# Kernel optimization log

Hardware: AMD Instinct MI355X
Metric: run time of the kernel (lower is better)

## Reference

```python
import jax, jax.numpy as jnp
import numpy as np

DIM = 512
HEADS = 8
EPS = 1e-5


def layer_norm(x, g, b):
    mu = jnp.mean(x, axis=-1, keepdims=True)
    var = jnp.mean(jnp.square(x - mu), axis=-1, keepdims=True)
    return (x - mu) * jax.lax.rsqrt(var + EPS) * g + b


def setup_inputs() -> dict:
    key = jax.random.key(0)
    ks = jax.random.split(key, 8)
    d = DIM
    s = 0.02
    return {
        "x": jax.random.normal(ks[0], (2, d, 64, 64), jnp.float32),
        "ln1_g": jnp.ones((d,), jnp.float32),
        "ln1_b": jnp.zeros((d,), jnp.float32),
        "w_qkv": jax.random.normal(ks[1], (d, 3 * d), jnp.float32) * s,
        "b_qkv": jnp.zeros((3 * d,), jnp.float32),
        "w_proj": jax.random.normal(ks[2], (d, d), jnp.float32) * s,
        "b_proj": jnp.zeros((d,), jnp.float32),
        "ln2_g": jnp.ones((d,), jnp.float32),
        "ln2_b": jnp.zeros((d,), jnp.float32),
        "w_ffn1": jax.random.normal(ks[3], (d, 4 * d), jnp.float32) * s,
        "b_ffn1": jnp.zeros((4 * d,), jnp.float32),
        "w_ffn2": jax.random.normal(ks[4], (4 * d, d), jnp.float32) * s,
        "b_ffn2": jnp.zeros((d,), jnp.float32),
    }


def reference(x, ln1_g, ln1_b, w_qkv, b_qkv, w_proj, b_proj,
              ln2_g, ln2_b, w_ffn1, b_ffn1, w_ffn2, b_ffn2):
    B, C, H, W = x.shape
    hd = C // HEADS
    x_in = x
    t = x.reshape(B, C, H * W).transpose(0, 2, 1)  # [B, N, C]
    h = layer_norm(t, ln1_g, ln1_b)
    qkv = h @ w_qkv + b_qkv  # [B, N, 3C]
    q, k, v = jnp.split(qkv, 3, axis=-1)
    def to_heads(a):
        return a.reshape(B, -1, HEADS, hd).transpose(0, 2, 1, 3)  # [B, h, N, hd]
    q, k, v = to_heads(q), to_heads(k), to_heads(v)
    # NOTE: module scales by 1/sqrt(C), not 1/sqrt(head_dim)
    attn = jnp.einsum('bhqd,bhkd->bhqk', q, k) / jnp.sqrt(jnp.float32(C))
    attn = jax.nn.softmax(attn, axis=-1)
    out = jnp.einsum('bhqk,bhkd->bhqd', attn, v)
    out = out.transpose(0, 2, 1, 3).reshape(B, -1, C)
    out = out @ w_proj + b_proj
    t = t + out
    h2 = layer_norm(t, ln2_g, ln2_b)
    ffn = jax.nn.relu(h2 @ w_ffn1 + b_ffn1) @ w_ffn2 + b_ffn2
    t = t + ffn
    y = t.transpose(0, 2, 1).reshape(B, C, H, W)
    return y + x_in
```

## Files before the change

kernel.cpp:

```cpp
#include <hip/hip_runtime.h>
#include <hip/hip_bf16.h>

typedef __bf16 bf16;
typedef __bf16 bf16x8 __attribute__((ext_vector_type(8)));
typedef __bf16 bf16x4 __attribute__((ext_vector_type(4)));
typedef float f32x4 __attribute__((ext_vector_type(4)));
typedef int int4v __attribute__((ext_vector_type(4)));
typedef int int2v __attribute__((ext_vector_type(2)));

#define DEV static __device__ __forceinline__

DEV void gload16(const void* g, void* l) {
    __builtin_amdgcn_global_load_lds(
        (const __attribute__((address_space(1))) void*)g,
        (__attribute__((address_space(3))) void*)l, 16, 0, 0);
}

DEV f32x4 mfma16(bf16x8 a, bf16x8 b, f32x4 c) {
    return __builtin_amdgcn_mfma_f32_16x16x32_bf16(a, b, c, 0, 0, 0);
}

DEV int cvtpk(float lo, float hi) {
    int r;
    asm("v_cvt_pk_bf16_f32 %0, %1, %2" : "=v"(r) : "v"(lo), "v"(hi));
    return r;
}

DEV float rexp2(float x) {
    float r;
    asm("v_exp_f32 %0, %1" : "=v"(r) : "v"(x));
    return r;
}

__global__ __launch_bounds__(256)
void k_transpose_x(const float* __restrict__ x, float* __restrict__ t) {
    __shared__ float tile[32][33];
    int bid = blockIdx.x;
    int nt = bid & 127, ct = (bid >> 7) & 15, b = bid >> 11;
    int n0 = nt * 32, c0 = ct * 32;
    int tid = threadIdx.x;
    const float* xb = x + (size_t)b * 512 * 4096;
    int nl = tid & 31, cl = tid >> 5;
#pragma unroll
    for (int i = 0; i < 4; i++) {
        int c = cl + i * 8;
        tile[c][nl] = xb[(size_t)(c0 + c) * 4096 + n0 + nl];
    }
    __syncthreads();
    float* tb = t + (size_t)b * 4096 * 512;
    int cl2 = tid & 31, nl2 = tid >> 5;
#pragma unroll
    for (int i = 0; i < 4; i++) {
        int n = nl2 + i * 8;
        tb[(size_t)(n0 + n) * 512 + c0 + cl2] = tile[cl2][n];
    }
}

__global__ __launch_bounds__(256)
void k_out3(const float* __restrict__ t, const bf16* __restrict__ f2o,
            const float* __restrict__ x, float* __restrict__ y) {
    __shared__ float tile[32][33];
    int bid = blockIdx.x;
    int nt = bid & 127, ct = (bid >> 7) & 15, b = bid >> 11;
    int n0 = nt * 32, c0 = ct * 32;
    int tid = threadIdx.x;
#pragma unroll
    for (int i = 0; i < 4; i++) {
        int nl = (tid >> 5) + i * 8;
        size_t idx = (size_t)(b * 4096 + n0 + nl) * 512 + c0 + (tid & 31);
        tile[tid & 31][nl] = t[idx] + (float)f2o[idx];
    }
    __syncthreads();
    const float* xb = x + ((size_t)b * 512 + c0) * 4096;
    float* yb = y + ((size_t)b * 512 + c0) * 4096;
#pragma unroll
    for (int i = 0; i < 4; i++) {
        int cl = (tid >> 5) + i * 8;
        int nl = tid & 31;
        size_t off = (size_t)cl * 4096 + n0 + nl;
        yb[off] = tile[cl][nl] + xb[off];
    }
}

__global__ __launch_bounds__(256)
void k_ln(const float* __restrict__ t, const float* __restrict__ gg,
          const float* __restrict__ bb, bf16* __restrict__ h) {
    int lane = threadIdx.x & 63;
    int row = blockIdx.x * 4 + (threadIdx.x >> 6);
    const float* tr = t + (size_t)row * 512;
    f32x4 v0 = *(const f32x4*)(tr + lane * 4);
    f32x4 v1 = *(const f32x4*)(tr + 256 + lane * 4);
    float s = v0[0] + v0[1] + v0[2] + v0[3] + v1[0] + v1[1] + v1[2] + v1[3];
#pragma unroll
    for (int m = 1; m < 64; m <<= 1) s += __shfl_xor(s, m);
    float mu = s * (1.0f / 512.0f);
    float vs = 0.f;
#pragma unroll
    for (int j = 0; j < 4; j++) {
        float d0 = v0[j] - mu, d1 = v1[j] - mu;
        vs += d0 * d0 + d1 * d1;
    }
#pragma unroll
    for (int m = 1; m < 64; m <<= 1) vs += __shfl_xor(vs, m);
    float rs = rsqrtf(vs * (1.0f / 512.0f) + 1e-5f);
    f32x4 g0 = *(const f32x4*)(gg + lane * 4);
    f32x4 g1 = *(const f32x4*)(gg + 256 + lane * 4);
    f32x4 b0 = *(const f32x4*)(bb + lane * 4);
    f32x4 b1 = *(const f32x4*)(bb + 256 + lane * 4);
    bf16x4 o0, o1;
#pragma unroll
    for (int j = 0; j < 4; j++) {
        o0[j] = (bf16)((v0[j] - mu) * rs * g0[j] + b0[j]);
        o1[j] = (bf16)((v1[j] - mu) * rs * g1[j] + b1[j]);
    }
    *(bf16x4*)(h + (size_t)row * 512 + lane * 4) = o0;
    *(bf16x4*)(h + (size_t)row * 512 + 256 + lane * 4) = o1;
}

__global__ __launch_bounds__(256)
void k_lnr(float* __restrict__ t, const bf16* __restrict__ r,
           const float* __restrict__ gg, const float* __restrict__ bb,
           bf16* __restrict__ h) {
    int lane = threadIdx.x & 63;
    int row = blockIdx.x * 4 + (threadIdx.x >> 6);
    float* tr = t + (size_t)row * 512;
    f32x4 v0 = *(const f32x4*)(tr + lane * 4);
    f32x4 v1 = *(const f32x4*)(tr + 256 + lane * 4);
    bf16x4 r0 = *(const bf16x4*)(r + (size_t)row * 512 + lane * 4);
    bf16x4 r1 = *(const bf16x4*)(r + (size_t)row * 512 + 256 + lane * 4);
#pragma unroll
    for (int j = 0; j < 4; j++) {
        v0[j] += (float)r0[j];
        v1[j] += (float)r1[j];
    }
    *(f32x4*)(tr + lane * 4) = v0;
    *(f32x4*)(tr + 256 + lane * 4) = v1;
    float s = v0[0] + v0[1] + v0[2] + v0[3] + v1[0] + v1[1] + v1[2] + v1[3];
#pragma unroll
    for (int m = 1; m < 64; m <<= 1) s += __shfl_xor(s, m);
    float mu = s * (1.0f / 512.0f);
    float vs = 0.f;
#pragma unroll
    for (int j = 0; j < 4; j++) {
        float d0 = v0[j] - mu, d1 = v1[j] - mu;
        vs += d0 * d0 + d1 * d1;
    }
#pragma unroll
    for (int m = 1; m < 64; m <<= 1) vs += __shfl_xor(vs, m);
    float rs = rsqrtf(vs * (1.0f / 512.0f) + 1e-5f);
    f32x4 g0 = *(const f32x4*)(gg + lane * 4);
    f32x4 g1 = *(const f32x4*)(gg + 256 + lane * 4);
    f32x4 b0 = *(const f32x4*)(bb + lane * 4);
    f32x4 b1 = *(const f32x4*)(bb + 256 + lane * 4);
    bf16x4 o0, o1;
#pragma unroll
    for (int j = 0; j < 4; j++) {
        o0[j] = (bf16)((v0[j] - mu) * rs * g0[j] + b0[j]);
        o1[j] = (bf16)((v1[j] - mu) * rs * g1[j] + b1[j]);
    }
    *(bf16x4*)(h + (size_t)row * 512 + lane * 4) = o0;
    *(bf16x4*)(h + (size_t)row * 512 + 256 + lane * 4) = o1;
}

__global__ __launch_bounds__(256)
void k_wt(const float* __restrict__ w, bf16* __restrict__ wt, int K, int N) {
    __shared__ float tile[32][33];
    int ntn = N >> 5;
    int kt = blockIdx.x / ntn, ntile = blockIdx.x % ntn;
    int k0 = kt * 32, n0 = ntile * 32;
    int tid = threadIdx.x;
    int nl = tid & 31, kl = tid >> 5;
#pragma unroll
    for (int i = 0; i < 4; i++) {
        int k = kl + i * 8;
        tile[k][nl] = w[(size_t)(k0 + k) * N + n0 + nl];
    }
    __syncthreads();
    int kl2 = tid & 31, nl2 = tid >> 5;
#pragma unroll
    for (int i = 0; i < 4; i++) {
        int n = nl2 + i * 8;
        wt[(size_t)(n0 + n) * K + k0 + kl2] = (bf16)tile[kl2][n];
    }
}

template <int MODE>
__global__ __launch_bounds__(256, 2)
void k_gemm(const bf16* __restrict__ A, const bf16* __restrict__ BT,
            const float* __restrict__ bias, bf16* __restrict__ outb,
            bf16* __restrict__ vtout, int M, int N, int K) {
    __shared__ char smem[65536];
    int ntn = N >> 7;
    int nwg = gridDim.x;
    int bid = blockIdx.x;
    int cpx = nwg >> 3;
    bid = (bid & 7) * cpx + (bid >> 3);
    int bm = bid / ntn, bn = bid % ntn;
    int m0 = bm * 128, n0 = bn * 128;
    int tid = threadIdx.x;
    int w = tid >> 6, l = tid & 63;
    int wm = w >> 1, wn = w & 1;
    int l15 = l & 15, lg = l >> 4;

    f32x4 acc[4][4];
#pragma unroll
    for (int i = 0; i < 4; i++)
#pragma unroll
        for (int j = 0; j < 4; j++) acc[i][j] = (f32x4){0.f, 0.f, 0.f, 0.f};

    int srow = tid >> 3, sphys = tid & 7;
    int lrow_a = wm * 64 + l15;
    int lrow_b = wn * 64 + l15;

#define GEMM_STAGE(k0v, bb)                                                  \
    do {                                                                     \
        _Pragma("unroll") for (int s = 0; s < 4; s++) {                      \
            int row = s * 32 + srow;                                         \
            int k16 = sphys ^ (row & 7);                                     \
            gload16(A + (size_t)(m0 + row) * K + (k0v) + k16 * 8,            \
                    smem + (bb) * 16384 + s * 4096 + tid * 16);              \
            gload16(BT + (size_t)(n0 + row) * K + (k0v) + k16 * 8,           \
                    smem + 32768 + (bb) * 16384 + s * 4096 + tid * 16);      \
        }                                                                    \
    } while (0)

    int nk = K >> 6;
    GEMM_STAGE(0, 0);
    int cur = 0;
    for (int kt = 0; kt < nk; kt++) {
        if (kt + 1 < nk) {
            GEMM_STAGE((kt + 1) << 6, cur ^ 1);
            asm volatile("s_waitcnt vmcnt(8)" ::: "memory");
        } else {
            asm volatile("s_waitcnt vmcnt(0)" ::: "memory");
        }
        __builtin_amdgcn_s_barrier();
        __builtin_amdgcn_sched_barrier(0);
        const char* pA = smem + cur * 16384;
        const char* pB = smem + 32768 + cur * 16384;
#pragma unroll
        for (int ks = 0; ks < 2; ks++) {
            bf16x8 af[4], bfr[4];
#pragma unroll
            for (int rg = 0; rg < 4; rg++) {
                int row = lrow_a + rg * 16;
                af[rg] = *(const bf16x8*)(pA + row * 128 +
                                          (((lg + ks * 4) ^ (row & 7)) << 4));
            }
#pragma unroll
            for (int cg = 0; cg < 4; cg++) {
                int row = lrow_b + cg * 16;
                bfr[cg] = *(const bf16x8*)(pB + row * 128 +
                                           (((lg + ks * 4) ^ (row & 7)) << 4));
            }
#pragma unroll
            for (int rg = 0; rg < 4; rg++)
#pragma unroll
                for (int cg = 0; cg < 4; cg++)
                    acc[rg][cg] = mfma16(af[rg], bfr[cg], acc[rg][cg]);
        }
        __builtin_amdgcn_s_barrier();
        cur ^= 1;
    }
#undef GEMM_STAGE

    if (MODE == 2 && n0 >= 1024) {
        char* vl = smem;
#pragma unroll
        for (int cg = 0; cg < 4; cg++) {
            int col = wn * 64 + cg * 16 + l15;
            float bz = bias[n0 + col];
#pragma unroll
            for (int rg = 0; rg < 4; rg++) {
                int rowb = wm * 64 + rg * 16 + lg * 4;
                int2v qq = {cvtpk(acc[rg][cg][0] + bz, acc[rg][cg][1] + bz),
                            cvtpk(acc[rg][cg][2] + bz, acc[rg][cg][3] + bz)};
                *(int2v*)(vl + col * 272 + rowb * 2) = qq;
            }
        }
        __syncthreads();
        int b = m0 >> 12, nrow0 = m0 & 4095;
        int dl = tid >> 3, c8 = tid & 7;
#pragma unroll
        for (int dd = 0; dd < 4; dd++) {
            int d = dd * 32 + dl;
            int ch = (n0 - 1024) + d;
            bf16* dst = vtout +
                ((size_t)((b * 8 + (ch >> 6)) * 64 + (ch & 63))) * 4096 + nrow0;
#pragma unroll
            for (int half = 0; half < 2; half++) {
                int chunk = half * 8 + c8;
                bf16x8 vv = *(const bf16x8*)(vl + d * 272 + chunk * 16);
                *(bf16x8*)(dst + chunk * 8) = vv;
            }
        }
        return;
    }

    char* ep = smem;
#pragma unroll
    for (int cg = 0; cg < 4; cg++) {
        int lcol = wn * 64 + cg * 16 + l15;
        float bz = bias[n0 + lcol];
#pragma unroll
        for (int rg = 0; rg < 4; rg++) {
#pragma unroll
            for (int j = 0; j < 4; j++) {
                int lrow = wm * 64 + rg * 16 + lg * 4 + j;
                float v = acc[rg][cg][j] + bz;
                if (MODE == 1) v = fmaxf(v, 0.f);
                *(bf16*)(ep + lrow * 264 + lcol * 2) = (bf16)v;
            }
        }
    }
    __syncthreads();
    int cch = tid & 15, rof = tid >> 4;
#pragma unroll
    for (int i = 0; i < 8; i++) {
        int row = i * 16 + rof;
        bf16x8 vv = *(const bf16x8*)(ep + row * 264 + cch * 16);
        *(bf16x8*)(outb + (size_t)(m0 + row) * N + n0 + cch * 8) = vv;
    }
}

__global__ __launch_bounds__(256, 4)
void k_attn(const bf16* __restrict__ qkvb, const bf16* __restrict__ vt,
            bf16* __restrict__ attno) {
    __shared__ bf16 sK[2][64 * 64];
    __shared__ bf16 sV[2][64 * 64];
    const float sc = 0.044194173824159216f * 1.4426950408889634f;
    int bid = blockIdx.x;
    int nb = (bid & 7) * 128 + (bid >> 3);
    int bh = nb >> 6, qt = nb & 63;
    int b = bh >> 3, hh = bh & 7;
    int q0 = qt * 64;
    int tid = threadIdx.x, w = tid >> 6, l = tid & 63;
    int l15 = l & 15, lg = l >> 4, l7 = l15 & 7;
    int lg4 = lg * 4;
    int vperm = ((lg & 1) << 1) | (lg >> 1);
    const bf16* qbase = qkvb + (size_t)b * 4096 * 1536 + hh * 64;
    const bf16* kbase = qbase + 512;
    const bf16* vbase = vt + (size_t)bh * 64 * 4096;
    int srow = tid >> 3, sphys = tid & 7;

    const char* kp0 = (const char*)&sK[0][0] + l15 * 128 + ((lg ^ l7) << 4);
    const char* kp1 = (const char*)&sK[0][0] + l15 * 128 + (((4 + lg) ^ l7) << 4);
    const char* vp0 = (const char*)&sV[0][0] + l15 * 128 + ((vperm ^ l7) << 4);
    const char* vp1 = (const char*)&sV[0][0] + l15 * 128 + (((4 + vperm) ^ l7) << 4);
    char* dK0 = (char*)&sK[0][0] + tid * 16;
    char* dV0 = (char*)&sV[0][0] + tid * 16;
    const char* kg = (const char*)(kbase + srow * 1536 + (sphys ^ (srow & 7)) * 8);
    const char* vg = (const char*)(vbase + srow * 4096 + (sphys ^ (srow & 7)) * 8);

    gload16(kg, dK0);
    gload16(kg + 98304, dK0 + 4096);
    gload16(vg, dV0);
    gload16(vg + 262144, dV0 + 4096);
    kg += 196608;
    vg += 128;

    bf16x8 qf[2];
#pragma unroll
    for (int ks = 0; ks < 2; ks++) {
        bf16x8 v = *(const bf16x8*)(qbase +
            (size_t)(q0 + w * 16 + l15) * 1536 + ks * 32 + lg * 8);
        bf16x8 o;
#pragma unroll
        for (int j = 0; j < 8; j++) o[j] = (bf16)((float)v[j] * sc);
        qf[ks] = o;
    }

    float lsum = 0.f;
    f32x4 acc[4];
#pragma unroll
    for (int df = 0; df < 4; df++) acc[df] = (f32x4){0.f, 0.f, 0.f, 0.f};

#define ABODY(BUF, PF)                                                        \
    {                                                                         \
        if (PF) {                                                             \
            gload16(kg, dK0 + (1 - (BUF)) * 8192);                            \
            gload16(kg + 98304, dK0 + (1 - (BUF)) * 8192 + 4096);             \
            gload16(vg, dV0 + (1 - (BUF)) * 8192);                            \
            gload16(vg + 262144, dV0 + (1 - (BUF)) * 8192 + 4096);            \
            kg += 196608;                                                     \
            vg += 128;                                                        \
            asm volatile("s_waitcnt vmcnt(4)" ::: "memory");                  \
        } else {                                                              \
            asm volatile("s_waitcnt vmcnt(0)" ::: "memory");                  \
        }                                                                     \
        __builtin_amdgcn_s_barrier();                                         \
        __builtin_amdgcn_sched_barrier(0);                                    \
        f32x4 s0 = {0.f, 0.f, 0.f, 0.f}, s1 = s0, s2 = s0, s3 = s0;           \
        __builtin_amdgcn_s_setprio(1);                                        \
        s0 = mfma16(*(const bf16x8*)(kp0 + (BUF) * 8192 + 0 * 2048), qf[0], s0); \
        s1 = mfma16(*(const bf16x8*)(kp0 + (BUF) * 8192 + 1 * 2048), qf[0], s1); \
        s2 = mfma16(*(const bf16x8*)(kp0 + (BUF) * 8192 + 2 * 2048), qf[0], s2); \
        s3 = mfma16(*(const bf16x8*)(kp0 + (BUF) * 8192 + 3 * 2048), qf[0], s3); \
        s0 = mfma16(*(const bf16x8*)(kp1 + (BUF) * 8192 + 0 * 2048), qf[1], s0); \
        s1 = mfma16(*(const bf16x8*)(kp1 + (BUF) * 8192 + 1 * 2048), qf[1], s1); \
        s2 = mfma16(*(const bf16x8*)(kp1 + (BUF) * 8192 + 2 * 2048), qf[1], s2); \
        s3 = mfma16(*(const bf16x8*)(kp1 + (BUF) * 8192 + 3 * 2048), qf[1], s3); \
        __builtin_amdgcn_s_setprio(0);                                        \
        float e0 = rexp2(s0[0]), e1 = rexp2(s0[1]);                           \
        float e2 = rexp2(s0[2]), e3 = rexp2(s0[3]);                           \
        float e4 = rexp2(s1[0]), e5 = rexp2(s1[1]);                           \
        float e6 = rexp2(s1[2]), e7 = rexp2(s1[3]);                           \
        float e8 = rexp2(s2[0]), e9 = rexp2(s2[1]);                           \
        float e10 = rexp2(s2[2]), e11 = rexp2(s2[3]);                         \
        float e12 = rexp2(s3[0]), e13 = rexp2(s3[1]);                         \
        float e14 = rexp2(s3[2]), e15 = rexp2(s3[3]);                         \
        lsum += (((e0 + e1) + (e2 + e3)) + ((e4 + e5) + (e6 + e7))) +         \
                (((e8 + e9) + (e10 + e11)) + ((e12 + e13) + (e14 + e15)));    \
        int p0 = cvtpk(e0, e1), p1 = cvtpk(e2, e3);                           \
        int p2 = cvtpk(e4, e5), p3 = cvtpk(e6, e7);                           \
        int p4 = cvtpk(e8, e9), p5 = cvtpk(e10, e11);                         \
        int p6 = cvtpk(e12, e13), p7 = cvtpk(e14, e15);                       \
        asm("v_permlane16_swap_b32 %0, %1" : "+v"(p2), "+v"(p0));             \
        asm("v_permlane16_swap_b32 %0, %1" : "+v"(p3), "+v"(p1));             \
        asm("v_permlane16_swap_b32 %0, %1" : "+v"(p6), "+v"(p4));             \
        asm("v_permlane16_swap_b32 %0, %1" : "+v"(p7), "+v"(p5));             \
        {                                                                     \
            int4v ai = {p0, p1, p2, p3};                                      \
            bf16x8 af = __builtin_bit_cast(bf16x8, ai);                       \
            __builtin_amdgcn_s_setprio(1);                                    \
            acc[0] = mfma16(af, *(const bf16x8*)(vp0 + (BUF) * 8192 + 0 * 2048), acc[0]); \
            acc[1] = mfma16(af, *(const bf16x8*)(vp0 + (BUF) * 8192 + 1 * 2048), acc[1]); \
            acc[2] = mfma16(af, *(const bf16x8*)(vp0 + (BUF) * 8192 + 2 * 2048), acc[2]); \
            acc[3] = mfma16(af, *(const bf16x8*)(vp0 + (BUF) * 8192 + 3 * 2048), acc[3]); \
        }                                                                     \
        {                                                                     \
            int4v ai = {p4, p5, p6, p7};                                      \
            bf16x8 af = __builtin_bit_cast(bf16x8, ai);                       \
            acc[0] = mfma16(af, *(const bf16x8*)(vp1 + (BUF) * 8192 + 0 * 2048), acc[0]); \
            acc[1] = mfma16(af, *(const bf16x8*)(vp1 + (BUF) * 8192 + 1 * 2048), acc[1]); \
            acc[2] = mfma16(af, *(const bf16x8*)(vp1 + (BUF) * 8192 + 2 * 2048), acc[2]); \
            acc[3] = mfma16(af, *(const bf16x8*)(vp1 + (BUF) * 8192 + 3 * 2048), acc[3]); \
            __builtin_amdgcn_s_setprio(0);                                    \
        }                                                                     \
        __builtin_amdgcn_s_barrier();                                         \
    }

    for (int tt = 0; tt < 31; tt++) {
        ABODY(0, 1)
        ABODY(1, 1)
    }
    ABODY(0, 1)
    ABODY(1, 0)
#undef ABODY

    lsum += __shfl_xor(lsum, 16);
    lsum += __shfl_xor(lsum, 32);
    float invq[4];
#pragma unroll
    for (int j = 0; j < 4; j++)
        invq[j] = 1.0f / __shfl(lsum, lg4 + j);

    bf16* ow = (bf16*)&sK[0][0] + w * 16 * 64;
#pragma unroll
    for (int df = 0; df < 4; df++) {
        int chunk = df * 2 + (l15 >> 3);
        int within = l15 & 7;
#pragma unroll
        for (int j = 0; j < 4; j++) {
            int q = lg * 4 + j;
            *(bf16*)((char*)ow + q * 128 + ((chunk ^ (q & 7)) << 4) + within * 2) =
                (bf16)(acc[df][j] * invq[j]);
        }
    }
    __syncthreads();
    const char* owr = (const char*)ow;
#pragma unroll
    for (int half = 0; half < 2; half++) {
        int r = l >> 2, ch = (l & 3) + half * 4;
        bf16x8 vv = *(const bf16x8*)(owr + r * 128 + ((ch ^ (r & 7)) << 4));
        *(bf16x8*)(attno + (size_t)(b * 4096 + q0 + w * 16 + r) * 512 +
                   hh * 64 + ch * 8) = vv;
    }
}

extern "C" void kernel_launch(void* const* d_in, const int* in_sizes, int n_in,
                              void* d_out, int out_size, void* d_ws, size_t ws_size,
                              hipStream_t stream) {
    const float* x = (const float*)d_in[0];
    const float* ln1g = (const float*)d_in[1];
    const float* ln1b = (const float*)d_in[2];
    const float* wqkv = (const float*)d_in[3];
    const float* bqkv = (const float*)d_in[4];
    const float* wproj = (const float*)d_in[5];
    const float* bproj = (const float*)d_in[6];
    const float* ln2g = (const float*)d_in[7];
    const float* ln2b = (const float*)d_in[8];
    const float* wffn1 = (const float*)d_in[9];
    const float* bffn1 = (const float*)d_in[10];
    const float* wffn2 = (const float*)d_in[11];
    const float* bffn2 = (const float*)d_in[12];
    float* y = (float*)d_out;

    char* ws = (char*)d_ws;
    float* t    = (float*)(ws + 0);
    bf16* h     = (bf16*)(ws + 16777216);
    bf16* qkvb  = (bf16*)(ws + 25165824);
    bf16* vtb   = (bf16*)(ws + 50331648);
    bf16* f1    = (bf16*)(ws + 25165824);
    bf16* wqT   = (bf16*)(ws + 58720256);
    bf16* wpT   = (bf16*)(ws + 60293120);
    bf16* w1T   = (bf16*)(ws + 60817408);
    bf16* w2T   = (bf16*)(ws + 62914560);
    bf16* attno = h;
    bf16* po    = vtb;
    bf16* f2o   = h;

    k_transpose_x<<<4096, 256, 0, stream>>>(x, t);
    k_ln<<<2048, 256, 0, stream>>>(t, ln1g, ln1b, h);
    k_wt<<<(512 / 32) * (1536 / 32), 256, 0, stream>>>(wqkv, wqT, 512, 1536);
    k_wt<<<(512 / 32) * (512 / 32), 256, 0, stream>>>(wproj, wpT, 512, 512);
    k_wt<<<(512 / 32) * (2048 / 32), 256, 0, stream>>>(wffn1, w1T, 512, 2048);
    k_wt<<<(2048 / 32) * (512 / 32), 256, 0, stream>>>(wffn2, w2T, 2048, 512);

    k_gemm<2><<<768, 256, 0, stream>>>(h, wqT, bqkv, qkvb, vtb, 8192, 1536, 512);
    k_attn<<<1024, 256, 0, stream>>>(qkvb, vtb, attno);
    k_gemm<0><<<256, 256, 0, stream>>>(attno, wpT, bproj, po, nullptr, 8192, 512, 512);
    k_lnr<<<2048, 256, 0, stream>>>(t, po, ln2g, ln2b, h);
    k_gemm<1><<<1024, 256, 0, stream>>>(h, w1T, bffn1, f1, nullptr, 8192, 2048, 512);
    k_gemm<0><<<256, 256, 0, stream>>>(f1, w2T, bffn2, f2o, nullptr, 8192, 512, 2048);
    k_out3<<<4096, 256, 0, stream>>>(t, f2o, x, y);
}
```

Measured before the change: 203.7 us.

## Triple-buffer attention with software-pipelined QK and 64-wide GEMM tiles for N=512

The attention kernel moves to a three-stage LDS ring and software-pipelines the loop, so the QK^T MFMAs for tile i+1 are issued before the softmax and PV of tile i. This lets exp work overlap with matrix work and keeps two prefetches in flight. Occupancy drops from 4 to 3 blocks per CU because of the larger shared buffer. Separately, the GEMM gains a BN template parameter, and the two N=512 GEMMs use 128x64 tiles with twice the workgroups, to fill the CUs better with only 256 tiles.

```diff
diff --git a/kernel.cpp b/kernel.cpp
--- a/kernel.cpp
+++ b/kernel.cpp
@@ -184,33 +184,34 @@
     }
 }
 
-template <int MODE>
+template <int MODE, int BN>
 __global__ __launch_bounds__(256, 2)
 void k_gemm(const bf16* __restrict__ A, const bf16* __restrict__ BT,
             const float* __restrict__ bias, bf16* __restrict__ outb,
             bf16* __restrict__ vtout, int M, int N, int K) {
     __shared__ char smem[65536];
-    int ntn = N >> 7;
+    constexpr int CG = BN / 32;
+    int ntn = N / BN;
     int nwg = gridDim.x;
     int bid = blockIdx.x;
     int cpx = nwg >> 3;
     bid = (bid & 7) * cpx + (bid >> 3);
     int bm = bid / ntn, bn = bid % ntn;
-    int m0 = bm * 128, n0 = bn * 128;
+    int m0 = bm * 128, n0 = bn * BN;
     int tid = threadIdx.x;
     int w = tid >> 6, l = tid & 63;
     int wm = w >> 1, wn = w & 1;
     int l15 = l & 15, lg = l >> 4;
 
-    f32x4 acc[4][4];
+    f32x4 acc[4][CG];
 #pragma unroll
     for (int i = 0; i < 4; i++)
 #pragma unroll
-        for (int j = 0; j < 4; j++) acc[i][j] = (f32x4){0.f, 0.f, 0.f, 0.f};
+        for (int j = 0; j < CG; j++) acc[i][j] = (f32x4){0.f, 0.f, 0.f, 0.f};
 
     int srow = tid >> 3, sphys = tid & 7;
     int lrow_a = wm * 64 + l15;
-    int lrow_b = wn * 64 + l15;
+    int lrow_b = wn * (BN / 2) + l15;
 
 #define GEMM_STAGE(k0v, bb)                                                  \
     do {                                                                     \
@@ -219,6 +220,10 @@
             int k16 = sphys ^ (row & 7);                                     \
             gload16(A + (size_t)(m0 + row) * K + (k0v) + k16 * 8,            \
                     smem + (bb) * 16384 + s * 4096 + tid * 16);              \
+        }                                                                    \
+        _Pragma("unroll") for (int s = 0; s < CG; s++) {                     \
+            int row = s * 32 + srow;                                         \
+            int k16 = sphys ^ (row & 7);                                     \
             gload16(BT + (size_t)(n0 + row) * K + (k0v) + k16 * 8,           \
                     smem + 32768 + (bb) * 16384 + s * 4096 + tid * 16);      \
         }                                                                    \
@@ -230,7 +235,10 @@
     for (int kt = 0; kt < nk; kt++) {
         if (kt + 1 < nk) {
             GEMM_STAGE((kt + 1) << 6, cur ^ 1);
-            asm volatile("s_waitcnt vmcnt(8)" ::: "memory");
+            if constexpr (BN == 128)
+                asm volatile("s_waitcnt vmcnt(8)" ::: "memory");
+            else
+                asm volatile("s_waitcnt vmcnt(6)" ::: "memory");
         } else {
             asm volatile("s_waitcnt vmcnt(0)" ::: "memory");
         }
@@ -240,7 +248,7 @@
         const char* pB = smem + 32768 + cur * 16384;
 #pragma unroll
         for (int ks = 0; ks < 2; ks++) {
-            bf16x8 af[4], bfr[4];
+            bf16x8 af[4], bfr[CG];
 #pragma unroll
             for (int rg = 0; rg < 4; rg++) {
                 int row = lrow_a + rg * 16;
@@ -248,7 +256,7 @@
                                           (((lg + ks * 4) ^ (row & 7)) << 4));
             }
 #pragma unroll
-            for (int cg = 0; cg < 4; cg++) {
+            for (int cg = 0; cg < CG; cg++) {
                 int row = lrow_b + cg * 16;
                 bfr[cg] = *(const bf16x8*)(pB + row * 128 +
                                            (((lg + ks * 4) ^ (row & 7)) << 4));
@@ -256,7 +264,7 @@
 #pragma unroll
             for (int rg = 0; rg < 4; rg++)
 #pragma unroll
-                for (int cg = 0; cg < 4; cg++)
+                for (int cg = 0; cg < CG; cg++)
                     acc[rg][cg] = mfma16(af[rg], bfr[cg], acc[rg][cg]);
         }
         __builtin_amdgcn_s_barrier();
@@ -264,43 +272,47 @@
     }
 #undef GEMM_STAGE
 
-    if (MODE == 2 && n0 >= 1024) {
-        char* vl = smem;
-#pragma unroll
-        for (int cg = 0; cg < 4; cg++) {
-            int col = wn * 64 + cg * 16 + l15;
-            float bz = bias[n0 + col];
-#pragma unroll
-            for (int rg = 0; rg < 4; rg++) {
-                int rowb = wm * 64 + rg * 16 + lg * 4;
-                int2v qq = {cvtpk(acc[rg][cg][0] + bz, acc[rg][cg][1] + bz),
-                            cvtpk(acc[rg][cg][2] + bz, acc[rg][cg][3] + bz)};
-                *(int2v*)(vl + col * 272 + rowb * 2) = qq;
+    if constexpr (MODE == 2) {
+        if (n0 >= 1024) {
+            char* vl = smem;
+#pragma unroll
+            for (int cg = 0; cg < CG; cg++) {
+                int col = wn * 64 + cg * 16 + l15;
+                float bz = bias[n0 + col];
+#pragma unroll
+                for (int rg = 0; rg < 4; rg++) {
+                    int rowb = wm * 64 + rg * 16 + lg * 4;
+                    int2v qq = {cvtpk(acc[rg][cg][0] + bz, acc[rg][cg][1] + bz),
+                                cvtpk(acc[rg][cg][2] + bz, acc[rg][cg][3] + bz)};
+                    *(int2v*)(vl + col * 272 + rowb * 2) = qq;
+                }
             }
+            __syncthreads();
+            int b = m0 >> 12, nrow0 = m0 & 4095;
+            int dl = tid >> 3, c8 = tid & 7;
+#pragma unroll
+            for (int dd = 0; dd < 4; dd++) {
+                int d = dd * 32 + dl;
+                int ch = (n0 - 1024) + d;
+                bf16* dst = vtout +
+                    ((size_t)((b * 8 + (ch >> 6)) * 64 + (ch & 63))) * 4096 + nrow0;
+#pragma unroll
+                for (int half = 0; half < 2; half++) {
+                    int chunk = half * 8 + c8;
+                    bf16x8 vv = *(const bf16x8*)(vl + d * 272 + chunk * 16);
+                    *(bf16x8*)(dst + chunk * 8) = vv;
+                }
+            }
+            return;
         }
-        __syncthreads();
-        int b = m0 >> 12, nrow0 = m0 & 4095;
-        int dl = tid >> 3, c8 = tid & 7;
-#pragma unroll
-        for (int dd = 0; dd < 4; dd++) {
-            int d = dd * 32 + dl;
-            int ch = (n0 - 1024) + d;
-            bf16* dst = vtout +
-                ((size_t)((b * 8 + (ch >> 6)) * 64 + (ch & 63))) * 4096 + nrow0;
-#pragma unroll
-            for (int half = 0; half < 2; half++) {
-                int chunk = half * 8 + c8;
-                bf16x8 vv = *(const bf16x8*)(vl + d * 272 + chunk * 16);
-                *(bf16x8*)(dst + chunk * 8) = vv;
-            }
-        }
-        return;
-    }
-
+    }
+
+    constexpr int RS = BN * 2 + 8;
+    constexpr int CH = BN / 8;
     char* ep = smem;
 #pragma unroll
-    for (int cg = 0; cg < 4; cg++) {
-        int lcol = wn * 64 + cg * 16 + l15;
+    for (int cg = 0; cg < CG; cg++) {
+        int lcol = wn * (BN / 2) + cg * 16 + l15;
         float bz = bias[n0 + lcol];
 #pragma unroll
         for (int rg = 0; rg < 4; rg++) {
@@ -309,25 +321,26 @@
                 int lrow = wm * 64 + rg * 16 + lg * 4 + j;
                 float v = acc[rg][cg][j] + bz;
                 if (MODE == 1) v = fmaxf(v, 0.f);
-                *(bf16*)(ep + lrow * 264 + lcol * 2) = (bf16)v;
+                *(bf16*)(ep + lrow * RS + lcol * 2) = (bf16)v;
             }
         }
     }
     __syncthreads();
-    int cch = tid & 15, rof = tid >> 4;
-#pragma unroll
-    for (int i = 0; i < 8; i++) {
-        int row = i * 16 + rof;
-        bf16x8 vv = *(const bf16x8*)(ep + row * 264 + cch * 16);
+    int cch = tid & (CH - 1);
+    int rof = tid / CH;
+    constexpr int RPP = 256 / CH;
+#pragma unroll
+    for (int i = 0; i < 128 / RPP; i++) {
+        int row = i * RPP + rof;
+        bf16x8 vv = *(const bf16x8*)(ep + row * RS + cch * 16);
         *(bf16x8*)(outb + (size_t)(m0 + row) * N + n0 + cch * 8) = vv;
     }
 }
 
-__global__ __launch_bounds__(256, 4)
+__global__ __launch_bounds__(256, 3)
 void k_attn(const bf16* __restrict__ qkvb, const bf16* __restrict__ vt,
             bf16* __restrict__ attno) {
-    __shared__ bf16 sK[2][64 * 64];
-    __shared__ bf16 sV[2][64 * 64];
+    __shared__ char sL[49152];
     const float sc = 0.044194173824159216f * 1.4426950408889634f;
     int bid = blockIdx.x;
     int nb = (bid & 7) * 128 + (bid >> 3);
@@ -343,21 +356,14 @@
     const bf16* vbase = vt + (size_t)bh * 64 * 4096;
     int srow = tid >> 3, sphys = tid & 7;
 
-    const char* kp0 = (const char*)&sK[0][0] + l15 * 128 + ((lg ^ l7) << 4);
-    const char* kp1 = (const char*)&sK[0][0] + l15 * 128 + (((4 + lg) ^ l7) << 4);
-    const char* vp0 = (const char*)&sV[0][0] + l15 * 128 + ((vperm ^ l7) << 4);
-    const char* vp1 = (const char*)&sV[0][0] + l15 * 128 + (((4 + vperm) ^ l7) << 4);
-    char* dK0 = (char*)&sK[0][0] + tid * 16;
-    char* dV0 = (char*)&sV[0][0] + tid * 16;
+    const char* kp0 = sL + l15 * 128 + ((lg ^ l7) << 4);
+    const char* kp1 = sL + l15 * 128 + (((4 + lg) ^ l7) << 4);
+    const char* vp0 = sL + 8192 + l15 * 128 + ((vperm ^ l7) << 4);
+    const char* vp1 = sL + 8192 + l15 * 128 + (((4 + vperm) ^ l7) << 4);
+    char* dK = sL + tid * 16;
+    char* dV = sL + 8192 + tid * 16;
     const char* kg = (const char*)(kbase + srow * 1536 + (sphys ^ (srow & 7)) * 8);
     const char* vg = (const char*)(vbase + srow * 4096 + (sphys ^ (srow & 7)) * 8);
-
-    gload16(kg, dK0);
-    gload16(kg + 98304, dK0 + 4096);
-    gload16(vg, dV0);
-    gload16(vg + 262144, dV0 + 4096);
-    kg += 196608;
-    vg += 128;
 
     bf16x8 qf[2];
 #pragma unroll
@@ -369,46 +375,50 @@
         for (int j = 0; j < 8; j++) o[j] = (bf16)((float)v[j] * sc);
         qf[ks] = o;
     }
-
+    asm volatile("s_waitcnt vmcnt(0)" ::: "memory");
+
+#define STG(BS)                                                               \
+    do {                                                                      \
+        gload16(kg, dK + (BS) * 16384);                                       \
+        gload16(kg + 98304, dK + (BS) * 16384 + 4096);                        \
+        gload16(vg, dV + (BS) * 16384);                                       \
+        gload16(vg + 262144, dV + (BS) * 16384 + 4096);                       \
+        kg += 196608;                                                         \
+        vg += 128;                                                            \
+    } while (0)
+
+    STG(0);
+    STG(1);
+
+    const f32x4 kZ = {0.f, 0.f, 0.f, 0.f};
+    f32x4 sE[4], sO[4];
     float lsum = 0.f;
     f32x4 acc[4];
 #pragma unroll
     for (int df = 0; df < 4; df++) acc[df] = (f32x4){0.f, 0.f, 0.f, 0.f};
 
-#define ABODY(BUF, PF)                                                        \
+#define QKC(SN, BQ)                                                           \
+    __builtin_amdgcn_s_setprio(1);                                            \
+    SN[0] = mfma16(*(const bf16x8*)(kp0 + (BQ) * 16384 + 0 * 2048), qf[0], kZ); \
+    SN[1] = mfma16(*(const bf16x8*)(kp0 + (BQ) * 16384 + 1 * 2048), qf[0], kZ); \
+    SN[2] = mfma16(*(const bf16x8*)(kp0 + (BQ) * 16384 + 2 * 2048), qf[0], kZ); \
+    SN[3] = mfma16(*(const bf16x8*)(kp0 + (BQ) * 16384 + 3 * 2048), qf[0], kZ); \
+    SN[0] = mfma16(*(const bf16x8*)(kp1 + (BQ) * 16384 + 0 * 2048), qf[1], SN[0]); \
+    SN[1] = mfma16(*(const bf16x8*)(kp1 + (BQ) * 16384 + 1 * 2048), qf[1], SN[1]); \
+    SN[2] = mfma16(*(const bf16x8*)(kp1 + (BQ) * 16384 + 2 * 2048), qf[1], SN[2]); \
+    SN[3] = mfma16(*(const bf16x8*)(kp1 + (BQ) * 16384 + 3 * 2048), qf[1], SN[3]); \
+    __builtin_amdgcn_s_setprio(0);
+
+#define SOFTPV(SOld, BP)                                                      \
     {                                                                         \
-        if (PF) {                                                             \
-            gload16(kg, dK0 + (1 - (BUF)) * 8192);                            \
-            gload16(kg + 98304, dK0 + (1 - (BUF)) * 8192 + 4096);             \
-            gload16(vg, dV0 + (1 - (BUF)) * 8192);                            \
-            gload16(vg + 262144, dV0 + (1 - (BUF)) * 8192 + 4096);            \
-            kg += 196608;                                                     \
-            vg += 128;                                                        \
-            asm volatile("s_waitcnt vmcnt(4)" ::: "memory");                  \
-        } else {                                                              \
-            asm volatile("s_waitcnt vmcnt(0)" ::: "memory");                  \
-        }                                                                     \
-        __builtin_amdgcn_s_barrier();                                         \
-        __builtin_amdgcn_sched_barrier(0);                                    \
-        f32x4 s0 = {0.f, 0.f, 0.f, 0.f}, s1 = s0, s2 = s0, s3 = s0;           \
-        __builtin_amdgcn_s_setprio(1);                                        \
-        s0 = mfma16(*(const bf16x8*)(kp0 + (BUF) * 8192 + 0 * 2048), qf[0], s0); \
-        s1 = mfma16(*(const bf16x8*)(kp0 + (BUF) * 8192 + 1 * 2048), qf[0], s1); \
-        s2 = mfma16(*(const bf16x8*)(kp0 + (BUF) * 8192 + 2 * 2048), qf[0], s2); \
-        s3 = mfma16(*(const bf16x8*)(kp0 + (BUF) * 8192 + 3 * 2048), qf[0], s3); \
-        s0 = mfma16(*(const bf16x8*)(kp1 + (BUF) * 8192 + 0 * 2048), qf[1], s0); \
-        s1 = mfma16(*(const bf16x8*)(kp1 + (BUF) * 8192 + 1 * 2048), qf[1], s1); \
-        s2 = mfma16(*(const bf16x8*)(kp1 + (BUF) * 8192 + 2 * 2048), qf[1], s2); \
-        s3 = mfma16(*(const bf16x8*)(kp1 + (BUF) * 8192 + 3 * 2048), qf[1], s3); \
-        __builtin_amdgcn_s_setprio(0);                                        \
-        float e0 = rexp2(s0[0]), e1 = rexp2(s0[1]);                           \
-        float e2 = rexp2(s0[2]), e3 = rexp2(s0[3]);                           \
-        float e4 = rexp2(s1[0]), e5 = rexp2(s1[1]);                           \
-        float e6 = rexp2(s1[2]), e7 = rexp2(s1[3]);                           \
-        float e8 = rexp2(s2[0]), e9 = rexp2(s2[1]);                           \
-        float e10 = rexp2(s2[2]), e11 = rexp2(s2[3]);                         \
-        float e12 = rexp2(s3[0]), e13 = rexp2(s3[1]);                         \
-        float e14 = rexp2(s3[2]), e15 = rexp2(s3[3]);                         \
+        float e0 = rexp2(SOld[0][0]), e1 = rexp2(SOld[0][1]);                 \
+        float e2 = rexp2(SOld[0][2]), e3 = rexp2(SOld[0][3]);                 \
+        float e4 = rexp2(SOld[1][0]), e5 = rexp2(SOld[1][1]);                 \
+        float e6 = rexp2(SOld[1][2]), e7 = rexp2(SOld[1][3]);                 \
+        float e8 = rexp2(SOld[2][0]), e9 = rexp2(SOld[2][1]);                 \
+        float e10 = rexp2(SOld[2][2]), e11 = rexp2(SOld[2][3]);               \
+        float e12 = rexp2(SOld[3][0]), e13 = rexp2(SOld[3][1]);               \
+        float e14 = rexp2(SOld[3][2]), e15 = rexp2(SOld[3][3]);               \
         lsum += (((e0 + e1) + (e2 + e3)) + ((e4 + e5) + (e6 + e7))) +         \
                 (((e8 + e9) + (e10 + e11)) + ((e12 + e13) + (e14 + e15)));    \
         int p0 = cvtpk(e0, e1), p1 = cvtpk(e2, e3);                           \
@@ -423,30 +433,58 @@
             int4v ai = {p0, p1, p2, p3};                                      \
             bf16x8 af = __builtin_bit_cast(bf16x8, ai);                       \
             __builtin_amdgcn_s_setprio(1);                                    \
-            acc[0] = mfma16(af, *(const bf16x8*)(vp0 + (BUF) * 8192 + 0 * 2048), acc[0]); \
-            acc[1] = mfma16(af, *(const bf16x8*)(vp0 + (BUF) * 8192 + 1 * 2048), acc[1]); \
-            acc[2] = mfma16(af, *(const bf16x8*)(vp0 + (BUF) * 8192 + 2 * 2048), acc[2]); \
-            acc[3] = mfma16(af, *(const bf16x8*)(vp0 + (BUF) * 8192 + 3 * 2048), acc[3]); \
+            acc[0] = mfma16(af, *(const bf16x8*)(vp0 + (BP) * 16384 + 0 * 2048), acc[0]); \
+            acc[1] = mfma16(af, *(const bf16x8*)(vp0 + (BP) * 16384 + 1 * 2048), acc[1]); \
+            acc[2] = mfma16(af, *(const bf16x8*)(vp0 + (BP) * 16384 + 2 * 2048), acc[2]); \
+            acc[3] = mfma16(af, *(const bf16x8*)(vp0 + (BP) * 16384 + 3 * 2048), acc[3]); \
         }                                                                     \
         {                                                                     \
             int4v ai = {p4, p5, p6, p7};                                      \
             bf16x8 af = __builtin_bit_cast(bf16x8, ai);                       \
-            acc[0] = mfma16(af, *(const bf16x8*)(vp1 + (BUF) * 8192 + 0 * 2048), acc[0]); \
-            acc[1] = mfma16(af, *(const bf16x8*)(vp1 + (BUF) * 8192 + 1 * 2048), acc[1]); \
-            acc[2] = mfma16(af, *(const bf16x8*)(vp1 + (BUF) * 8192 + 2 * 2048), acc[2]); \
-            acc[3] = mfma16(af, *(const bf16x8*)(vp1 + (BUF) * 8192 + 3 * 2048), acc[3]); \
+            acc[0] = mfma16(af, *(const bf16x8*)(vp1 + (BP) * 16384 + 0 * 2048), acc[0]); \
+            acc[1] = mfma16(af, *(const bf16x8*)(vp1 + (BP) * 16384 + 1 * 2048), acc[1]); \
+            acc[2] = mfma16(af, *(const bf16x8*)(vp1 + (BP) * 16384 + 2 * 2048), acc[2]); \
+            acc[3] = mfma16(af, *(const bf16x8*)(vp1 + (BP) * 16384 + 3 * 2048), acc[3]); \
             __builtin_amdgcn_s_setprio(0);                                    \
         }                                                                     \
+    }
+
+#define BODY(BS, BQ, SN, SOld, BP, PF)                                        \
+    {                                                                         \
+        if (PF) {                                                             \
+            STG(BS);                                                          \
+            asm volatile("s_waitcnt vmcnt(4)" ::: "memory");                  \
+        } else {                                                              \
+            asm volatile("s_waitcnt vmcnt(0)" ::: "memory");                  \
+        }                                                                     \
         __builtin_amdgcn_s_barrier();                                         \
-    }
-
-    for (int tt = 0; tt < 31; tt++) {
-        ABODY(0, 1)
-        ABODY(1, 1)
-    }
-    ABODY(0, 1)
-    ABODY(1, 0)
-#undef ABODY
+        __builtin_amdgcn_sched_barrier(0);                                    \
+        QKC(SN, BQ)                                                           \
+        SOFTPV(SOld, BP)                                                      \
+        __builtin_amdgcn_s_barrier();                                         \
+    }
+
+    asm volatile("s_waitcnt vmcnt(4)" ::: "memory");
+    __builtin_amdgcn_s_barrier();
+    __builtin_amdgcn_sched_barrier(0);
+    QKC(sE, 0)
+
+    for (int tt = 0; tt < 10; tt++) {
+        BODY(2, 1, sO, sE, 0, 1)
+        BODY(0, 2, sE, sO, 1, 1)
+        BODY(1, 0, sO, sE, 2, 1)
+        BODY(2, 1, sE, sO, 0, 1)
+        BODY(0, 2, sO, sE, 1, 1)
+        BODY(1, 0, sE, sO, 2, 1)
+    }
+    BODY(2, 1, sO, sE, 0, 1)
+    BODY(0, 2, sE, sO, 1, 1)
+    BODY(1, 0, sO, sE, 2, 0)
+    SOFTPV(sO, 0)
+#undef BODY
+#undef SOFTPV
+#undef QKC
+#undef STG
 
     lsum += __shfl_xor(lsum, 16);
     lsum += __shfl_xor(lsum, 32);
@@ -455,7 +493,8 @@
     for (int j = 0; j < 4; j++)
         invq[j] = 1.0f / __shfl(lsum, lg4 + j);
 
-    bf16* ow = (bf16*)&sK[0][0] + w * 16 * 64;
+    __syncthreads();
+    bf16* ow = (bf16*)sL + w * 16 * 64;
 #pragma unroll
     for (int df = 0; df < 4; df++) {
         int chunk = df * 2 + (l15 >> 3);
@@ -517,11 +556,11 @@
     k_wt<<<(512 / 32) * (2048 / 32), 256, 0, stream>>>(wffn1, w1T, 512, 2048);
     k_wt<<<(2048 / 32) * (512 / 32), 256, 0, stream>>>(wffn2, w2T, 2048, 512);
 
-    k_gemm<2><<<768, 256, 0, stream>>>(h, wqT, bqkv, qkvb, vtb, 8192, 1536, 512);
+    k_gemm<2, 128><<<768, 256, 0, stream>>>(h, wqT, bqkv, qkvb, vtb, 8192, 1536, 512);
     k_attn<<<1024, 256, 0, stream>>>(qkvb, vtb, attno);
-    k_gemm<0><<<256, 256, 0, stream>>>(attno, wpT, bproj, po, nullptr, 8192, 512, 512);
+    k_gemm<0, 64><<<512, 256, 0, stream>>>(attno, wpT, bproj, po, nullptr, 8192, 512, 512);
     k_lnr<<<2048, 256, 0, stream>>>(t, po, ln2g, ln2b, h);
-    k_gemm<1><<<1024, 256, 0, stream>>>(h, w1T, bffn1, f1, nullptr, 8192, 2048, 512);
-    k_gemm<0><<<256, 256, 0, stream>>>(f1, w2T, bffn2, f2o, nullptr, 8192, 512, 2048);
+    k_gemm<1, 128><<<1024, 256, 0, stream>>>(h, w1T, bffn1, f1, nullptr, 8192, 2048, 512);
+    k_gemm<0, 64><<<512, 256, 0, stream>>>(f1, w2T, bffn2, f2o, nullptr, 8192, 512, 2048);
     k_out3<<<4096, 256, 0, stream>>>(t, f2o, x, y);
 }
```

Measured after the change: 208.3 us. 2.2% more time.
